# Kernel optimization log

Measured on AMD Instinct MI355X. Metric: run time of the kernel, lower is better.

## Reference

```python
import jax, jax.numpy as jnp
import numpy as np
from jax import lax

B, C, T, H, W = 4, 3, 2, 64, 64
DIM, HEADS, DH, MLP, DEPTH, SR, RES = 192, 3, 64, 768, 2, 2, 64
INNER = HEADS * DH  # 192 == DIM
N = RES * RES + 1   # 4097 tokens (cls + patches)


def setup_inputs() -> dict:
    key = jax.random.key(0)
    ks = iter(jax.random.split(key, 64))
    def rn(shape, s=0.02):
        return jax.random.normal(next(ks), shape, jnp.float32) * s
    d = {}
    d["x"] = jax.random.normal(next(ks), (B, C, T, H, W), jnp.float32)
    # patch embed conv3d (kernel (1,1,1) since patch_size=1) + layernorm
    d["pe_w"] = rn((DIM, C, 1, 1, 1))
    d["pe_b"] = jnp.zeros((DIM,), jnp.float32)
    d["pe_ln_g"] = jnp.ones((DIM,), jnp.float32)
    d["pe_ln_b"] = jnp.zeros((DIM,), jnp.float32)
    d["pos_emb"] = rn((1, T, N, DIM), 1.0)      # torch.randn
    d["space_token"] = rn((1, 1, DIM), 1.0)     # torch.randn
    ones2 = jnp.ones((DEPTH, DIM), jnp.float32)
    zeros2 = jnp.zeros((DEPTH, DIM), jnp.float32)
    # space transformer (Sattention with SR conv)
    d["s_ln1_g"], d["s_ln1_b"] = ones2, zeros2
    d["s_wq"] = rn((DEPTH, INNER, DIM))
    d["s_wkv"] = rn((DEPTH, 2 * INNER, DIM))
    d["s_wo"] = rn((DEPTH, DIM, INNER))
    d["s_bo"] = jnp.zeros((DEPTH, DIM), jnp.float32)
    d["s_sr_w"] = rn((DEPTH, DIM, DIM, SR, SR))
    d["s_sr_b"] = jnp.zeros((DEPTH, DIM), jnp.float32)
    d["s_ln2_g"], d["s_ln2_b"] = ones2, zeros2
    d["s_w1"] = rn((DEPTH, MLP, DIM))
    d["s_b1"] = jnp.zeros((DEPTH, MLP), jnp.float32)
    d["s_w2"] = rn((DEPTH, DIM, MLP))
    d["s_b2"] = jnp.zeros((DEPTH, DIM), jnp.float32)
    d["s_lnf_g"] = jnp.ones((DIM,), jnp.float32)
    d["s_lnf_b"] = jnp.zeros((DIM,), jnp.float32)
    # temporal transformer (plain attention over t=2 cls tokens)
    d["t_ln1_g"], d["t_ln1_b"] = ones2, zeros2
    d["t_wqkv"] = rn((DEPTH, 3 * INNER, DIM))
    d["t_wo"] = rn((DEPTH, DIM, INNER))
    d["t_bo"] = jnp.zeros((DEPTH, DIM), jnp.float32)
    d["t_ln2_g"], d["t_ln2_b"] = ones2, zeros2
    d["t_w1"] = rn((DEPTH, MLP, DIM))
    d["t_b1"] = jnp.zeros((DEPTH, MLP), jnp.float32)
    d["t_w2"] = rn((DEPTH, DIM, MLP))
    d["t_b2"] = jnp.zeros((DEPTH, DIM), jnp.float32)
    d["t_lnf_g"] = jnp.ones((DIM,), jnp.float32)
    d["t_lnf_b"] = jnp.zeros((DIM,), jnp.float32)
    return d


def _ln(x, g, b, eps=1e-5):
    m = jnp.mean(x, -1, keepdims=True)
    v = jnp.var(x, -1, keepdims=True)
    return (x - m) * lax.rsqrt(v + eps) * g + b


def _heads(t):
    b, n, _ = t.shape
    return t.reshape(b, n, HEADS, DH).transpose(0, 2, 1, 3)  # b h n d


def _attend(q, k, v):
    dots = jnp.einsum('bhid,bhjd->bhij', q, k) * (DH ** -0.5)
    attn = jax.nn.softmax(dots, axis=-1)
    o = jnp.einsum('bhij,bhjd->bhid', attn, v)
    return o.transpose(0, 2, 1, 3).reshape(q.shape[0], q.shape[2], INNER)


def _ff(x, w1, b1, w2, b2):
    h = jax.nn.gelu(x @ w1.T + b1, approximate=False)
    return h @ w2.T + b2


def _sattn(x, wq, wkv, wo, bo, srw, srb):
    bn = x.shape[0]
    q = _heads(x @ wq.T)
    # spatial reduction of non-cls tokens: b n d -> b d h w, conv stride SR
    xs = x[:, 1:].transpose(0, 2, 1).reshape(bn, DIM, RES, RES)
    xs = lax.conv_general_dilated(xs, srw, (SR, SR), 'VALID',
                                  dimension_numbers=('NCHW', 'OIHW', 'NCHW'))
    xs = xs + srb[None, :, None, None]
    xs = xs.reshape(bn, DIM, -1).transpose(0, 2, 1)
    xk = jnp.concatenate([x[:, :1], xs], axis=1)   # prepend cls token
    kv = xk @ wkv.T
    k, v = _heads(kv[..., :INNER]), _heads(kv[..., INNER:])
    return _attend(q, k, v) @ wo.T + bo


def _attn(x, wqkv, wo, bo):
    qkv = x @ wqkv.T
    q = _heads(qkv[..., :INNER])
    k = _heads(qkv[..., INNER:2 * INNER])
    v = _heads(qkv[..., 2 * INNER:])
    return _attend(q, k, v) @ wo.T + bo


def reference(x, pe_w, pe_b, pe_ln_g, pe_ln_b, pos_emb, space_token,
              s_ln1_g, s_ln1_b, s_wq, s_wkv, s_wo, s_bo, s_sr_w, s_sr_b,
              s_ln2_g, s_ln2_b, s_w1, s_b1, s_w2, s_b2, s_lnf_g, s_lnf_b,
              t_ln1_g, t_ln1_b, t_wqkv, t_wo, t_bo, t_ln2_g, t_ln2_b,
              t_w1, t_b1, t_w2, t_b2, t_lnf_g, t_lnf_b):
    # patch embed: (b,c,t,h,w) -> (b,t,hw,dim) with layernorm
    y = lax.conv_general_dilated(x, pe_w, (1, 1, 1), 'VALID',
                                 dimension_numbers=('NCDHW', 'OIDHW', 'NCDHW'))
    y = y + pe_b[None, :, None, None, None]
    y = jnp.transpose(y, (0, 2, 3, 4, 1)).reshape(B, T, RES * RES, DIM)
    y = _ln(y, pe_ln_g, pe_ln_b)
    cls = jnp.broadcast_to(space_token[:, None], (B, T, 1, DIM))
    xx = jnp.concatenate([cls, y], axis=2) + pos_emb[:, :, :N]
    xx = xx.reshape(B * T, N, DIM)
    for i in range(DEPTH):
        xx = _sattn(_ln(xx, s_ln1_g[i], s_ln1_b[i]), s_wq[i], s_wkv[i],
                    s_wo[i], s_bo[i], s_sr_w[i], s_sr_b[i]) + xx
        xx = _ff(_ln(xx, s_ln2_g[i], s_ln2_b[i]), s_w1[i], s_b1[i],
                 s_w2[i], s_b2[i]) + xx
    xx = _ln(xx, s_lnf_g, s_lnf_b)
    out = xx[:, 1:].reshape(B, T, RES, RES, DIM)
    z = xx[:, 0].reshape(B, T, DIM)
    for i in range(DEPTH):
        z = _attn(_ln(z, t_ln1_g[i], t_ln1_b[i]), t_wqkv[i], t_wo[i], t_bo[i]) + z
        z = _ff(_ln(z, t_ln2_g[i], t_ln2_b[i]), t_w1[i], t_b1[i], t_w2[i], t_b2[i]) + z
    z = _ln(z, t_lnf_g, t_lnf_b)
    return out + out * z[:, :, None, None, :]
```

## Files before the change

kernel.cpp:

```cpp
#include <hip/hip_runtime.h>
#include <hip/hip_bf16.h>
#include <math.h>

typedef __hip_bfloat16 bf16;
typedef short bf16x8 __attribute__((ext_vector_type(8)));
typedef float f32x4  __attribute__((ext_vector_type(4)));

#define BATCH 4
#define TT 2
#define BT 8
#define DIM 192
#define NTOK 4097
#define NKTOK 1025
#define HEADS 3
#define DH 64
#define MLPD 768
#define RES 64

__device__ __forceinline__ float b2f(bf16 v) { return __bfloat162float(v); }

__device__ __forceinline__ float rload(const void* p, size_t i, int flag) {
    if (flag) return __bfloat162float(((const bf16*)p)[i]);
    return ((const float*)p)[i];
}

__global__ void detect_kernel(const void* probe, int* flag) {
    unsigned u = *(const unsigned*)probe;
    *flag = (u == 0x3F800000u) ? 0 : 1;
}

__device__ __forceinline__ float blk_reduce_192(float v, float* tmp) {
    #pragma unroll
    for (int m = 32; m > 0; m >>= 1) v += __shfl_xor(v, m, 64);
    int wid = threadIdx.x >> 6;
    if ((threadIdx.x & 63) == 0) tmp[wid] = v;
    __syncthreads();
    float s = tmp[0] + tmp[1] + tmp[2];
    __syncthreads();
    return s;
}

__global__ void patch_embed_kernel(const void* __restrict__ x, const void* __restrict__ pe_w,
                                   const void* __restrict__ pe_b, const void* __restrict__ lng,
                                   const void* __restrict__ lnb, const void* __restrict__ pos,
                                   const void* __restrict__ st, float* __restrict__ XX,
                                   const int* __restrict__ dflag) {
    __shared__ float tmp[3];
    int flag = *dflag;
    int blk = blockIdx.x;
    int bt = blk / NTOK, n = blk % NTOK;
    int b = bt >> 1, t = bt & 1;
    int d = threadIdx.x;
    float val;
    if (n == 0) {
        val = rload(st, d, flag);
    } else {
        int p = n - 1, h = p >> 6, w = p & 63;
        size_t base = (size_t)(b * 6 + t) * 4096 + h * 64 + w;
        float conv = rload(pe_b, d, flag);
        #pragma unroll
        for (int c = 0; c < 3; ++c)
            conv += rload(x, base + (size_t)c * TT * 4096, flag) * rload(pe_w, d * 3 + c, flag);
        float s = blk_reduce_192(conv, tmp);
        float mean = s * (1.f / 192.f);
        float dv = conv - mean;
        float s2 = blk_reduce_192(dv * dv, tmp);
        float var = s2 * (1.f / 192.f);
        val = dv * rsqrtf(var + 1e-5f) * rload(lng, d, flag) + rload(lnb, d, flag);
    }
    val += rload(pos, ((size_t)t * NTOK + n) * DIM + d, flag);
    XX[(size_t)blk * DIM + d] = val;
}

__global__ void ln_bf16_kernel(const float* __restrict__ X, const void* __restrict__ g,
                               const void* __restrict__ b, size_t goff, bf16* __restrict__ Y,
                               const int* __restrict__ dflag) {
    __shared__ float tmp[3];
    int flag = *dflag;
    size_t row = blockIdx.x;
    int d = threadIdx.x;
    float v = X[row * DIM + d];
    float s = blk_reduce_192(v, tmp);
    float mean = s * (1.f / 192.f);
    float dv = v - mean;
    float s2 = blk_reduce_192(dv * dv, tmp);
    float var = s2 * (1.f / 192.f);
    Y[row * DIM + d] = __float2bfloat16(dv * rsqrtf(var + 1e-5f) * rload(g, goff + d, flag)
                                        + rload(b, goff + d, flag));
}

__global__ void ln_f32_kernel(const float* __restrict__ X, const void* __restrict__ g,
                              const void* __restrict__ b, size_t goff, float* __restrict__ Y,
                              long in_stride, const int* __restrict__ dflag) {
    __shared__ float tmp[3];
    int flag = *dflag;
    int d = threadIdx.x;
    float v = X[(size_t)blockIdx.x * in_stride + d];
    float s = blk_reduce_192(v, tmp);
    float mean = s * (1.f / 192.f);
    float dv = v - mean;
    float s2 = blk_reduce_192(dv * dv, tmp);
    float var = s2 * (1.f / 192.f);
    Y[(size_t)blockIdx.x * DIM + d] = dv * rsqrtf(var + 1e-5f) * rload(g, goff + d, flag)
                                      + rload(b, goff + d, flag);
}

__global__ __launch_bounds__(256) void gemm_mfma_kernel(
        const bf16* __restrict__ A, const void* __restrict__ W, size_t woff,
        const void* __restrict__ bias, size_t boff, const float* __restrict__ resid,
        float* __restrict__ Cf, bf16* __restrict__ Cb,
        int M, int N, int K, int do_gelu, const int* __restrict__ dflag) {
    __shared__ __align__(16) bf16 As[64 * 32];
    __shared__ __align__(16) bf16 Bs[64 * 32];
    int flag = *dflag;
    int tid = threadIdx.x;
    int wave = tid >> 6, lane = tid & 63;
    int quad = lane >> 4, l16 = lane & 15;
    int rowBase = blockIdx.y * 64;
    int colBase = blockIdx.x * 64;
    int srow = tid >> 2, scol = (tid & 3) * 8;

    f32x4 acc0 = {0.f, 0.f, 0.f, 0.f};
    f32x4 acc1 = acc0, acc2 = acc0, acc3 = acc0;

    for (int k0 = 0; k0 < K; k0 += 32) {
        {
            int gr = rowBase + srow;
            uint4 v = make_uint4(0u, 0u, 0u, 0u);
            if (gr < M) v = *reinterpret_cast<const uint4*>(A + (size_t)gr * K + k0 + scol);
            *reinterpret_cast<uint4*>(&As[srow * 32 + scol]) = v;
        }
        {
            int gr = colBase + srow;
            if (flag) {
                uint4 v = *reinterpret_cast<const uint4*>((const bf16*)W + woff + (size_t)gr * K + k0 + scol);
                *reinterpret_cast<uint4*>(&Bs[srow * 32 + scol]) = v;
            } else {
                const float* wp = (const float*)W + woff + (size_t)gr * K + k0 + scol;
                bf16 tmp8[8];
                #pragma unroll
                for (int j = 0; j < 8; ++j) tmp8[j] = __float2bfloat16(wp[j]);
                *reinterpret_cast<uint4*>(&Bs[srow * 32 + scol]) = *reinterpret_cast<uint4*>(tmp8);
            }
        }
        __syncthreads();
        bf16x8 af = *reinterpret_cast<bf16x8*>(&As[(wave * 16 + l16) * 32 + quad * 8]);
        bf16x8 bf0 = *reinterpret_cast<bf16x8*>(&Bs[(0 * 16 + l16) * 32 + quad * 8]);
        bf16x8 bf1 = *reinterpret_cast<bf16x8*>(&Bs[(1 * 16 + l16) * 32 + quad * 8]);
        bf16x8 bf2 = *reinterpret_cast<bf16x8*>(&Bs[(2 * 16 + l16) * 32 + quad * 8]);
        bf16x8 bf3 = *reinterpret_cast<bf16x8*>(&Bs[(3 * 16 + l16) * 32 + quad * 8]);
        acc0 = __builtin_amdgcn_mfma_f32_16x16x32_bf16(af, bf0, acc0, 0, 0, 0);
        acc1 = __builtin_amdgcn_mfma_f32_16x16x32_bf16(af, bf1, acc1, 0, 0, 0);
        acc2 = __builtin_amdgcn_mfma_f32_16x16x32_bf16(af, bf2, acc2, 0, 0, 0);
        acc3 = __builtin_amdgcn_mfma_f32_16x16x32_bf16(af, bf3, acc3, 0, 0, 0);
        __syncthreads();
    }

    f32x4 accs[4] = {acc0, acc1, acc2, acc3};
    #pragma unroll
    for (int t = 0; t < 4; ++t) {
        int col = colBase + t * 16 + l16;
        float bv = bias ? rload(bias, boff + col, flag) : 0.f;
        #pragma unroll
        for (int r = 0; r < 4; ++r) {
            int row = rowBase + wave * 16 + quad * 4 + r;
            if (row < M) {
                float v = accs[t][r] + bv;
                if (do_gelu) v = 0.5f * v * (1.f + erff(v * 0.70710678118654752f));
                if (resid) v += resid[(size_t)row * N + col];
                if (Cf) Cf[(size_t)row * N + col] = v;
                else    Cb[(size_t)row * N + col] = __float2bfloat16(v);
            }
        }
    }
}

__global__ void gemm_fA_kernel(const float* __restrict__ A, const void* __restrict__ W,
                               size_t woff, const void* __restrict__ bias, size_t boff,
                               const float* __restrict__ resid, float* __restrict__ C,
                               int M, int N, int K, int do_gelu, const int* __restrict__ dflag) {
    __shared__ float As[16][17];
    __shared__ float Ws[16][17];
    int flag = *dflag;
    int tx = threadIdx.x, ty = threadIdx.y;
    int row = blockIdx.y * 16 + ty;
    int col = blockIdx.x * 16 + tx;
    float acc = 0.f;
    for (int k0 = 0; k0 < K; k0 += 16) {
        As[ty][tx] = (row < M) ? A[(size_t)row * K + k0 + tx] : 0.f;
        int wr = blockIdx.x * 16 + ty;
        Ws[ty][tx] = (wr < N) ? rload(W, woff + (size_t)wr * K + k0 + tx, flag) : 0.f;
        __syncthreads();
        #pragma unroll
        for (int kk = 0; kk < 16; ++kk)
            acc += As[ty][kk] * Ws[tx][kk];
        __syncthreads();
    }
    if (row < M && col < N) {
        float v = acc;
        if (bias) v += rload(bias, boff + col, flag);
        if (do_gelu) v = 0.5f * v * (1.f + erff(v * 0.70710678118654752f));
        if (resid) v += resid[(size_t)row * N + col];
        C[(size_t)row * N + col] = v;
    }
}

__global__ void copy_cls_kernel(const bf16* __restrict__ AB, bf16* __restrict__ XK) {
    int bt = blockIdx.x, d = threadIdx.x;
    XK[(size_t)bt * NKTOK * DIM + d] = AB[(size_t)bt * NTOK * DIM + d];
}

__global__ void wtrans_kernel(const void* __restrict__ srw, bf16* __restrict__ WT,
                              const int* __restrict__ dflag) {
    int flag = *dflag;
    int idx = blockIdx.x * 256 + threadIdx.x;
    int i = idx / (192 * 768);
    int rem = idx - i * (192 * 768);
    int dout = rem / 768;
    int kp = rem - dout * 768;
    int q = kp / 192, c = kp - q * 192;
    size_t src = ((size_t)(i * 192 + dout) * 192 + c) * 4 + q;
    WT[idx] = __float2bfloat16(rload(srw, src, flag));
}

__global__ __launch_bounds__(256) void srconv_mfma_kernel(
        const bf16* __restrict__ XLN, const bf16* __restrict__ WT, size_t woff,
        const void* __restrict__ bias, size_t boff, bf16* __restrict__ XK,
        const int* __restrict__ dflag) {
    __shared__ __align__(16) bf16 As[64 * 32];
    __shared__ __align__(16) bf16 Bs[64 * 32];
    int flag = *dflag;
    int tid = threadIdx.x;
    int wave = tid >> 6, lane = tid & 63;
    int quad = lane >> 4, l16 = lane & 15;
    int rowBase = blockIdx.y * 64;
    int colBase = blockIdx.x * 64;
    int srow = tid >> 2, scol = (tid & 3) * 8;

    int arow = rowBase + srow;
    int abt = arow >> 10, apos = arow & 1023;
    int aoh = apos >> 5, aow = apos & 31;

    f32x4 acc0 = {0.f, 0.f, 0.f, 0.f};
    f32x4 acc1 = acc0, acc2 = acc0, acc3 = acc0;

    for (int k0 = 0; k0 < 768; k0 += 32) {
        int q = k0 / 192, c0 = k0 - q * 192;
        int kh = q >> 1, kw = q & 1;
        int n = 1 + ((2 * aoh + kh) << 6) + (2 * aow + kw);
        {
            uint4 v = *reinterpret_cast<const uint4*>(
                XLN + ((size_t)abt * NTOK + n) * DIM + c0 + scol);
            *reinterpret_cast<uint4*>(&As[srow * 32 + scol]) = v;
        }
        {
            int gr = colBase + srow;
            uint4 v = *reinterpret_cast<const uint4*>(WT + woff + (size_t)gr * 768 + k0 + scol);
            *reinterpret_cast<uint4*>(&Bs[srow * 32 + scol]) = v;
        }
        __syncthreads();
        bf16x8 af = *reinterpret_cast<bf16x8*>(&As[(wave * 16 + l16) * 32 + quad * 8]);
        bf16x8 bf0 = *reinterpret_cast<bf16x8*>(&Bs[(0 * 16 + l16) * 32 + quad * 8]);
        bf16x8 bf1 = *reinterpret_cast<bf16x8*>(&Bs[(1 * 16 + l16) * 32 + quad * 8]);
        bf16x8 bf2 = *reinterpret_cast<bf16x8*>(&Bs[(2 * 16 + l16) * 32 + quad * 8]);
        bf16x8 bf3 = *reinterpret_cast<bf16x8*>(&Bs[(3 * 16 + l16) * 32 + quad * 8]);
        acc0 = __builtin_amdgcn_mfma_f32_16x16x32_bf16(af, bf0, acc0, 0, 0, 0);
        acc1 = __builtin_amdgcn_mfma_f32_16x16x32_bf16(af, bf1, acc1, 0, 0, 0);
        acc2 = __builtin_amdgcn_mfma_f32_16x16x32_bf16(af, bf2, acc2, 0, 0, 0);
        acc3 = __builtin_amdgcn_mfma_f32_16x16x32_bf16(af, bf3, acc3, 0, 0, 0);
        __syncthreads();
    }

    f32x4 accs[4] = {acc0, acc1, acc2, acc3};
    #pragma unroll
    for (int t = 0; t < 4; ++t) {
        int col = colBase + t * 16 + l16;
        float bv = rload(bias, boff + col, flag);
        #pragma unroll
        for (int r = 0; r < 4; ++r) {
            int row = rowBase + wave * 16 + quad * 4 + r;
            int bt = row >> 10, pos = row & 1023;
            XK[((size_t)bt * NKTOK + 1 + pos) * DIM + col] = __float2bfloat16(accs[t][r] + bv);
        }
    }
}

__global__ __launch_bounds__(256) void sattn_mfma_kernel(const bf16* __restrict__ Q,
                                                         const bf16* __restrict__ KV,
                                                         bf16* __restrict__ O) {
    __shared__ __align__(16) bf16 Ks[32 * 72];
    __shared__ __align__(16) bf16 Vts[64 * 36];
    __shared__ __align__(16) bf16 Ps[4][16 * 68];

    int bt = blockIdx.x / HEADS, h = blockIdx.x % HEADS;
    int q0 = blockIdx.y * 64;
    int tid = threadIdx.x;
    int wave = tid >> 6, lane = tid & 63;
    int quad = lane >> 4, l16 = lane & 15;

    int qrow = q0 + wave * 16 + l16;
    int qr = (qrow < NTOK) ? qrow : (NTOK - 1);
    const bf16* qp = Q + ((size_t)bt * NTOK + qr) * DIM + h * DH + quad * 8;
    bf16x8 aq0 = *reinterpret_cast<const bf16x8*>(qp);
    bf16x8 aq1 = *reinterpret_cast<const bf16x8*>(qp + 32);

    float l_r[4] = {0.f, 0.f, 0.f, 0.f};
    f32x4 O0 = {0.f, 0.f, 0.f, 0.f}, O1 = O0, O2 = O0, O3 = O0;

    int skey = tid & 31, sdh0 = (tid >> 5) * 8;
    union U8 { bf16x8 v; uint2 u[2]; };

    for (int kt0 = 0; kt0 < NKTOK; kt0 += 32) {
        __syncthreads();
        {
            int gkey = kt0 + skey;
            uint4 kv4 = make_uint4(0u, 0u, 0u, 0u), vv4 = make_uint4(0u, 0u, 0u, 0u);
            if (gkey < NKTOK) {
                const bf16* kp = KV + ((size_t)bt * NKTOK + gkey) * (2 * DIM) + h * DH + sdh0;
                kv4 = *reinterpret_cast<const uint4*>(kp);
                vv4 = *reinterpret_cast<const uint4*>(kp + DIM);
            }
            *reinterpret_cast<uint2*>(&Ks[skey * 72 + sdh0])     = make_uint2(kv4.x, kv4.y);
            *reinterpret_cast<uint2*>(&Ks[skey * 72 + sdh0 + 4]) = make_uint2(kv4.z, kv4.w);
            const bf16* vb = reinterpret_cast<const bf16*>(&vv4);
            #pragma unroll
            for (int j = 0; j < 8; ++j) Vts[(sdh0 + j) * 36 + skey] = vb[j];
        }
        __syncthreads();

        f32x4 S[2];
        #pragma unroll
        for (int sub = 0; sub < 2; ++sub) {
            U8 k0c, k1c;
            const bf16* kr = &Ks[(sub * 16 + l16) * 72 + quad * 8];
            k0c.u[0] = *reinterpret_cast<const uint2*>(kr);
            k0c.u[1] = *reinterpret_cast<const uint2*>(kr + 4);
            const bf16* kr2 = kr + 32;
            k1c.u[0] = *reinterpret_cast<const uint2*>(kr2);
            k1c.u[1] = *reinterpret_cast<const uint2*>(kr2 + 4);
            f32x4 z = {0.f, 0.f, 0.f, 0.f};
            z = __builtin_amdgcn_mfma_f32_16x16x32_bf16(aq0, k0c.v, z, 0, 0, 0);
            z = __builtin_amdgcn_mfma_f32_16x16x32_bf16(aq1, k1c.v, z, 0, 0, 0);
            S[sub] = z;
        }

        bool oob0 = (kt0 + l16) >= NKTOK;
        bool oob1 = (kt0 + 16 + l16) >= NKTOK;
        #pragma unroll
        for (int r = 0; r < 4; ++r) {
            float p0 = oob0 ? 0.f : __expf(S[0][r] * 0.125f);
            float p1 = oob1 ? 0.f : __expf(S[1][r] * 0.125f);
            l_r[r] += p0 + p1;
            Ps[wave][(quad * 4 + r) * 68 + l16]      = __float2bfloat16(p0);
            Ps[wave][(quad * 4 + r) * 68 + 16 + l16] = __float2bfloat16(p1);
        }

        U8 pa;
        const bf16* pp = &Ps[wave][l16 * 68 + quad * 8];
        pa.u[0] = *reinterpret_cast<const uint2*>(pp);
        pa.u[1] = *reinterpret_cast<const uint2*>(pp + 4);
        U8 vf[4];
        #pragma unroll
        for (int t = 0; t < 4; ++t) {
            const bf16* vp = &Vts[(t * 16 + l16) * 36 + quad * 8];
            vf[t].u[0] = *reinterpret_cast<const uint2*>(vp);
            vf[t].u[1] = *reinterpret_cast<const uint2*>(vp + 4);
        }
        O0 = __builtin_amdgcn_mfma_f32_16x16x32_bf16(pa.v, vf[0].v, O0, 0, 0, 0);
        O1 = __builtin_amdgcn_mfma_f32_16x16x32_bf16(pa.v, vf[1].v, O1, 0, 0, 0);
        O2 = __builtin_amdgcn_mfma_f32_16x16x32_bf16(pa.v, vf[2].v, O2, 0, 0, 0);
        O3 = __builtin_amdgcn_mfma_f32_16x16x32_bf16(pa.v, vf[3].v, O3, 0, 0, 0);
    }

    #pragma unroll
    for (int r = 0; r < 4; ++r) {
        #pragma unroll
        for (int msk = 1; msk < 16; msk <<= 1)
            l_r[r] += __shfl_xor(l_r[r], msk, 64);
    }

    f32x4 Os[4] = {O0, O1, O2, O3};
    #pragma unroll
    for (int r = 0; r < 4; ++r) {
        int row = q0 + wave * 16 + quad * 4 + r;
        if (row < NTOK) {
            float inv = 1.f / l_r[r];
            bf16* op = O + ((size_t)bt * NTOK + row) * DIM + h * DH + l16;
            #pragma unroll
            for (int t = 0; t < 4; ++t)
                op[t * 16] = __float2bfloat16(Os[t][r] * inv);
        }
    }
}

__global__ void tattn_kernel(const float* __restrict__ QKV, float* __restrict__ O) {
    int b = blockIdx.x / HEADS, h = blockIdx.x % HEADS;
    int d = threadIdx.x;
    int r0 = b * 2, r1 = b * 2 + 1;
    float q0 = QKV[r0 * 576 + h * DH + d];
    float q1 = QKV[r1 * 576 + h * DH + d];
    float k0 = QKV[r0 * 576 + 192 + h * DH + d];
    float k1 = QKV[r1 * 576 + 192 + h * DH + d];
    float v0 = QKV[r0 * 576 + 384 + h * DH + d];
    float v1 = QKV[r1 * 576 + 384 + h * DH + d];
    float s00 = q0 * k0, s01 = q0 * k1, s10 = q1 * k0, s11 = q1 * k1;
    #pragma unroll
    for (int mm = 32; mm > 0; mm >>= 1) {
        s00 += __shfl_xor(s00, mm, 64);
        s01 += __shfl_xor(s01, mm, 64);
        s10 += __shfl_xor(s10, mm, 64);
        s11 += __shfl_xor(s11, mm, 64);
    }
    s00 *= 0.125f; s01 *= 0.125f; s10 *= 0.125f; s11 *= 0.125f;
    float m0 = fmaxf(s00, s01), m1 = fmaxf(s10, s11);
    float e00 = expf(s00 - m0), e01 = expf(s01 - m0);
    float e10 = expf(s10 - m1), e11 = expf(s11 - m1);
    float i0 = 1.f / (e00 + e01), i1 = 1.f / (e10 + e11);
    O[r0 * DIM + h * DH + d] = (e00 * v0 + e01 * v1) * i0;
    O[r1 * DIM + h * DH + d] = (e10 * v0 + e11 * v1) * i1;
}

__global__ void final_kernel(const float* __restrict__ XX, const void* __restrict__ g,
                             const void* __restrict__ b, const float* __restrict__ ZF,
                             void* __restrict__ out, const int* __restrict__ dflag) {
    __shared__ float tmp[3];
    int flag = *dflag;
    int tok = blockIdx.x;
    int bt = tok >> 12, p = tok & 4095;
    int d = threadIdx.x;
    size_t row = (size_t)bt * NTOK + 1 + p;
    float v = XX[row * DIM + d];
    float s = blk_reduce_192(v, tmp);
    float mean = s * (1.f / 192.f);
    float dv = v - mean;
    float s2 = blk_reduce_192(dv * dv, tmp);
    float var = s2 * (1.f / 192.f);
    float ln = dv * rsqrtf(var + 1e-5f) * rload(g, d, flag) + rload(b, d, flag);
    float o = ln * (1.f + ZF[bt * DIM + d]);
    size_t oi = (size_t)tok * DIM + d;
    if (flag) ((bf16*)out)[oi] = __float2bfloat16(o);
    else      ((float*)out)[oi] = o;
}

extern "C" void kernel_launch(void* const* d_in, const int* in_sizes, int n_in,
                              void* d_out, int out_size, void* d_ws, size_t ws_size,
                              hipStream_t stream) {
    const void* x       = d_in[0];
    const void* pe_w    = d_in[1];
    const void* pe_b    = d_in[2];
    const void* pe_ln_g = d_in[3];
    const void* pe_ln_b = d_in[4];
    const void* pos_emb = d_in[5];
    const void* space_t = d_in[6];
    const void* s_ln1_g = d_in[7];
    const void* s_ln1_b = d_in[8];
    const void* s_wq    = d_in[9];
    const void* s_wkv   = d_in[10];
    const void* s_wo    = d_in[11];
    const void* s_bo    = d_in[12];
    const void* s_sr_w  = d_in[13];
    const void* s_sr_b  = d_in[14];
    const void* s_ln2_g = d_in[15];
    const void* s_ln2_b = d_in[16];
    const void* s_w1    = d_in[17];
    const void* s_b1    = d_in[18];
    const void* s_w2    = d_in[19];
    const void* s_b2    = d_in[20];
    const void* s_lnf_g = d_in[21];
    const void* s_lnf_b = d_in[22];
    const void* t_ln1_g = d_in[23];
    const void* t_ln1_b = d_in[24];
    const void* t_wqkv  = d_in[25];
    const void* t_wo    = d_in[26];
    const void* t_bo    = d_in[27];
    const void* t_ln2_g = d_in[28];
    const void* t_ln2_b = d_in[29];
    const void* t_w1    = d_in[30];
    const void* t_b1    = d_in[31];
    const void* t_w2    = d_in[32];
    const void* t_b2    = d_in[33];
    const void* t_lnf_g = d_in[34];
    const void* t_lnf_b = d_in[35];

    const int M  = BT * NTOK;
    const int MK = BT * NKTOK;
    const int CHROWS = 8194;

    char* base = (char*)d_ws;
    int* dflag = (int*)base;
    size_t off = 256;
    auto carve = [&](size_t bytes) -> void* {
        void* p = base + off;
        off += (bytes + 255) & ~(size_t)255;
        return p;
    };
    float* XX = (float*)carve((size_t)M * DIM * 4);
    bf16*  AB = (bf16*) carve((size_t)M * DIM * 2);
    bf16*  QH = (bf16*) carve((size_t)M * DIM * 2);
    bf16*  XK = (bf16*) carve((size_t)MK * DIM * 2);
    bf16*  KV = (bf16*) carve((size_t)MK * 2 * DIM * 2);
    bf16*  WT = (bf16*) carve((size_t)2 * DIM * 768 * 2);
    float* Z    = (float*)carve(BT * DIM * 4);
    float* ZLN  = (float*)carve(BT * DIM * 4);
    float* ZQKV = (float*)carve(BT * 576 * 4);
    float* ZATT = (float*)carve(BT * DIM * 4);
    float* ZH   = (float*)carve(BT * MLPD * 4);
    float* ZF   = (float*)carve(BT * DIM * 4);

    dim3 g16(16, 16);

    detect_kernel<<<1, 1, 0, stream>>>(pe_ln_g, dflag);
    wtrans_kernel<<<(2 * 192 * 768) / 256, 256, 0, stream>>>(s_sr_w, WT, dflag);
    patch_embed_kernel<<<M, DIM, 0, stream>>>(x, pe_w, pe_b, pe_ln_g, pe_ln_b,
                                              pos_emb, space_t, XX, dflag);

    for (int i = 0; i < 2; ++i) {
        size_t oLN  = (size_t)i * DIM;
        size_t oWQ  = (size_t)i * DIM * DIM;
        size_t oWKV = (size_t)i * 2 * DIM * DIM;
        size_t oWO  = (size_t)i * DIM * DIM;
        size_t oWT  = (size_t)i * DIM * 768;
        size_t oW1  = (size_t)i * MLPD * DIM;
        size_t oB1  = (size_t)i * MLPD;
        size_t oW2  = (size_t)i * DIM * MLPD;

        ln_bf16_kernel<<<M, DIM, 0, stream>>>(XX, s_ln1_g, s_ln1_b, oLN, AB, dflag);
        gemm_mfma_kernel<<<dim3(DIM / 64, (M + 63) / 64), 256, 0, stream>>>(
            AB, s_wq, oWQ, nullptr, 0, nullptr, nullptr, QH, M, DIM, DIM, 0, dflag);
        copy_cls_kernel<<<BT, DIM, 0, stream>>>(AB, XK);
        srconv_mfma_kernel<<<dim3(DIM / 64, (BT * 1024) / 64), 256, 0, stream>>>(
            AB, WT, oWT, s_sr_b, oLN, XK, dflag);
        gemm_mfma_kernel<<<dim3(2 * DIM / 64, (MK + 63) / 64), 256, 0, stream>>>(
            XK, s_wkv, oWKV, nullptr, 0, nullptr, nullptr, KV, MK, 2 * DIM, DIM, 0, dflag);
        sattn_mfma_kernel<<<dim3(BT * HEADS, (NTOK + 63) / 64), 256, 0, stream>>>(QH, KV, AB);
        gemm_mfma_kernel<<<dim3(DIM / 64, (M + 63) / 64), 256, 0, stream>>>(
            AB, s_wo, oWO, s_bo, oLN, XX, XX, nullptr, M, DIM, DIM, 0, dflag);
        ln_bf16_kernel<<<M, DIM, 0, stream>>>(XX, s_ln2_g, s_ln2_b, oLN, AB, dflag);
        for (int c = 0; c < 4; ++c) {
            size_t aoff = (size_t)c * CHROWS * DIM;
            gemm_mfma_kernel<<<dim3(MLPD / 64, (CHROWS + 63) / 64), 256, 0, stream>>>(
                AB + aoff, s_w1, oW1, s_b1, oB1, nullptr, nullptr, QH, CHROWS, MLPD, DIM, 1, dflag);
            gemm_mfma_kernel<<<dim3(DIM / 64, (CHROWS + 63) / 64), 256, 0, stream>>>(
                QH, s_w2, oW2, s_b2, oLN, XX + aoff, XX + aoff, nullptr, CHROWS, DIM, MLPD, 0, dflag);
        }
    }

    ln_f32_kernel<<<BT, DIM, 0, stream>>>(XX, s_lnf_g, s_lnf_b, 0, Z, (long)((size_t)NTOK * DIM), dflag);
    for (int i = 0; i < 2; ++i) {
        size_t oLN   = (size_t)i * DIM;
        size_t oWQKV = (size_t)i * 3 * DIM * DIM;
        size_t oWO   = (size_t)i * DIM * DIM;
        size_t oW1   = (size_t)i * MLPD * DIM;
        size_t oB1   = (size_t)i * MLPD;
        size_t oW2   = (size_t)i * DIM * MLPD;
        ln_f32_kernel<<<BT, DIM, 0, stream>>>(Z, t_ln1_g, t_ln1_b, oLN, ZLN, DIM, dflag);
        gemm_fA_kernel<<<dim3(576 / 16, 1), g16, 0, stream>>>(
            ZLN, t_wqkv, oWQKV, nullptr, 0, nullptr, ZQKV, BT, 576, DIM, 0, dflag);
        tattn_kernel<<<BATCH * HEADS, 64, 0, stream>>>(ZQKV, ZATT);
        gemm_fA_kernel<<<dim3(DIM / 16, 1), g16, 0, stream>>>(
            ZATT, t_wo, oWO, t_bo, oLN, Z, Z, BT, DIM, DIM, 0, dflag);
        ln_f32_kernel<<<BT, DIM, 0, stream>>>(Z, t_ln2_g, t_ln2_b, oLN, ZLN, DIM, dflag);
        gemm_fA_kernel<<<dim3(MLPD / 16, 1), g16, 0, stream>>>(
            ZLN, t_w1, oW1, t_b1, oB1, nullptr, ZH, BT, MLPD, DIM, 1, dflag);
        gemm_fA_kernel<<<dim3(DIM / 16, 1), g16, 0, stream>>>(
            ZH, t_w2, oW2, t_b2, oLN, Z, Z, BT, DIM, MLPD, 0, dflag);
    }
    ln_f32_kernel<<<BT, DIM, 0, stream>>>(Z, t_lnf_g, t_lnf_b, 0, ZF, DIM, dflag);

    final_kernel<<<BT * 4096, DIM, 0, stream>>>(XX, s_lnf_g, s_lnf_b, ZF, d_out, dflag);
}
```

Before: 1.029 ms.

## Fuse temporal transformer into one kernel and use wave-per-row layernorms

Replaces the chain of small temporal-transformer launches (layernorms, tiled fp32 GEMMs, attention) with one single-block kernel. That kernel keeps the 8 cls-token rows in shared memory and streams the weights with 8-wide vector loads. Layernorm, patch-embed and final kernels now process one row per 64-wide wave, four rows per block, with shuffle-only reductions, which removes the shared-memory reductions and __syncthreads. The goal is lower launch overhead and better occupancy, at the cost of running the temporal weight streaming on a single CU.

```diff
diff --git a/kernel.cpp b/kernel.cpp
--- a/kernel.cpp
+++ b/kernel.cpp
@@ -24,85 +24,103 @@
     return ((const float*)p)[i];
 }
 
+__device__ __forceinline__ void unpack8(uint4 u, float* f) {
+    unsigned w[4] = {u.x, u.y, u.z, u.w};
+    #pragma unroll
+    for (int k = 0; k < 4; ++k) {
+        union { unsigned u; float f; } a, b;
+        a.u = (w[k] & 0xFFFFu) << 16;
+        b.u = w[k] & 0xFFFF0000u;
+        f[2 * k] = a.f;
+        f[2 * k + 1] = b.f;
+    }
+}
+
+__device__ __forceinline__ void wload8(const void* W, size_t i, int flag, float* f) {
+    if (flag) {
+        uint4 u = *reinterpret_cast<const uint4*>((const bf16*)W + i);
+        unpack8(u, f);
+    } else {
+        const float* p = (const float*)W + i;
+        #pragma unroll
+        for (int j = 0; j < 8; ++j) f[j] = p[j];
+    }
+}
+
 __global__ void detect_kernel(const void* probe, int* flag) {
     unsigned u = *(const unsigned*)probe;
     *flag = (u == 0x3F800000u) ? 0 : 1;
 }
 
-__device__ __forceinline__ float blk_reduce_192(float v, float* tmp) {
-    #pragma unroll
-    for (int m = 32; m > 0; m >>= 1) v += __shfl_xor(v, m, 64);
-    int wid = threadIdx.x >> 6;
-    if ((threadIdx.x & 63) == 0) tmp[wid] = v;
-    __syncthreads();
-    float s = tmp[0] + tmp[1] + tmp[2];
-    __syncthreads();
-    return s;
-}
-
-__global__ void patch_embed_kernel(const void* __restrict__ x, const void* __restrict__ pe_w,
-                                   const void* __restrict__ pe_b, const void* __restrict__ lng,
-                                   const void* __restrict__ lnb, const void* __restrict__ pos,
-                                   const void* __restrict__ st, float* __restrict__ XX,
-                                   const int* __restrict__ dflag) {
-    __shared__ float tmp[3];
+__global__ __launch_bounds__(256) void patch_embed4_kernel(
+        const void* __restrict__ x, const void* __restrict__ pe_w,
+        const void* __restrict__ pe_b, const void* __restrict__ lng,
+        const void* __restrict__ lnb, const void* __restrict__ pos,
+        const void* __restrict__ st, float* __restrict__ XX,
+        const int* __restrict__ dflag) {
     int flag = *dflag;
-    int blk = blockIdx.x;
-    int bt = blk / NTOK, n = blk % NTOK;
+    int w = threadIdx.x >> 6, lane = threadIdx.x & 63;
+    int row = blockIdx.x * 4 + w;
+    int bt = row / NTOK, n = row % NTOK;
     int b = bt >> 1, t = bt & 1;
-    int d = threadIdx.x;
-    float val;
+    int d0 = lane, d1 = lane + 64, d2 = lane + 128;
+    float o0, o1, o2;
     if (n == 0) {
-        val = rload(st, d, flag);
+        o0 = rload(st, d0, flag); o1 = rload(st, d1, flag); o2 = rload(st, d2, flag);
     } else {
-        int p = n - 1, h = p >> 6, w = p & 63;
-        size_t base = (size_t)(b * 6 + t) * 4096 + h * 64 + w;
-        float conv = rload(pe_b, d, flag);
-        #pragma unroll
-        for (int c = 0; c < 3; ++c)
-            conv += rload(x, base + (size_t)c * TT * 4096, flag) * rload(pe_w, d * 3 + c, flag);
-        float s = blk_reduce_192(conv, tmp);
+        int p = n - 1, hh = p >> 6, ww = p & 63;
+        size_t base = (size_t)(b * 6 + t) * 4096 + hh * 64 + ww;
+        float xv0 = rload(x, base, flag);
+        float xv1 = rload(x, base + (size_t)TT * 4096, flag);
+        float xv2 = rload(x, base + (size_t)2 * TT * 4096, flag);
+        float c0 = rload(pe_b, d0, flag) + xv0 * rload(pe_w, d0 * 3, flag)
+                 + xv1 * rload(pe_w, d0 * 3 + 1, flag) + xv2 * rload(pe_w, d0 * 3 + 2, flag);
+        float c1 = rload(pe_b, d1, flag) + xv0 * rload(pe_w, d1 * 3, flag)
+                 + xv1 * rload(pe_w, d1 * 3 + 1, flag) + xv2 * rload(pe_w, d1 * 3 + 2, flag);
+        float c2 = rload(pe_b, d2, flag) + xv0 * rload(pe_w, d2 * 3, flag)
+                 + xv1 * rload(pe_w, d2 * 3 + 1, flag) + xv2 * rload(pe_w, d2 * 3 + 2, flag);
+        float s = c0 + c1 + c2;
+        #pragma unroll
+        for (int m = 32; m > 0; m >>= 1) s += __shfl_xor(s, m, 64);
         float mean = s * (1.f / 192.f);
-        float dv = conv - mean;
-        float s2 = blk_reduce_192(dv * dv, tmp);
-        float var = s2 * (1.f / 192.f);
-        val = dv * rsqrtf(var + 1e-5f) * rload(lng, d, flag) + rload(lnb, d, flag);
-    }
-    val += rload(pos, ((size_t)t * NTOK + n) * DIM + d, flag);
-    XX[(size_t)blk * DIM + d] = val;
-}
-
-__global__ void ln_bf16_kernel(const float* __restrict__ X, const void* __restrict__ g,
-                               const void* __restrict__ b, size_t goff, bf16* __restrict__ Y,
-                               const int* __restrict__ dflag) {
-    __shared__ float tmp[3];
+        float e0 = c0 - mean, e1 = c1 - mean, e2 = c2 - mean;
+        float s2 = e0 * e0 + e1 * e1 + e2 * e2;
+        #pragma unroll
+        for (int m = 32; m > 0; m >>= 1) s2 += __shfl_xor(s2, m, 64);
+        float inv = rsqrtf(s2 * (1.f / 192.f) + 1e-5f);
+        o0 = e0 * inv * rload(lng, d0, flag) + rload(lnb, d0, flag);
+        o1 = e1 * inv * rload(lng, d1, flag) + rload(lnb, d1, flag);
+        o2 = e2 * inv * rload(lng, d2, flag) + rload(lnb, d2, flag);
+    }
+    size_t pbase = ((size_t)t * NTOK + n) * DIM;
+    o0 += rload(pos, pbase + d0, flag);
+    o1 += rload(pos, pbase + d1, flag);
+    o2 += rload(pos, pbase + d2, flag);
+    float* xp = XX + (size_t)row * DIM;
+    xp[d0] = o0; xp[d1] = o1; xp[d2] = o2;
+}
+
+__global__ __launch_bounds__(256) void ln4_kernel(const float* __restrict__ X,
+        const void* __restrict__ g, const void* __restrict__ b, size_t goff,
+        bf16* __restrict__ Y, const int* __restrict__ dflag) {
     int flag = *dflag;
-    size_t row = blockIdx.x;
-    int d = threadIdx.x;
-    float v = X[row * DIM + d];
-    float s = blk_reduce_192(v, tmp);
+    int w = threadIdx.x >> 6, lane = threadIdx.x & 63;
+    size_t row = (size_t)blockIdx.x * 4 + w;
+    const float* xp = X + row * DIM;
+    float v0 = xp[lane], v1 = xp[lane + 64], v2 = xp[lane + 128];
+    float s = v0 + v1 + v2;
+    #pragma unroll
+    for (int m = 32; m > 0; m >>= 1) s += __shfl_xor(s, m, 64);
     float mean = s * (1.f / 192.f);
-    float dv = v - mean;
-    float s2 = blk_reduce_192(dv * dv, tmp);
-    float var = s2 * (1.f / 192.f);
-    Y[row * DIM + d] = __float2bfloat16(dv * rsqrtf(var + 1e-5f) * rload(g, goff + d, flag)
-                                        + rload(b, goff + d, flag));
-}
-
-__global__ void ln_f32_kernel(const float* __restrict__ X, const void* __restrict__ g,
-                              const void* __restrict__ b, size_t goff, float* __restrict__ Y,
-                              long in_stride, const int* __restrict__ dflag) {
-    __shared__ float tmp[3];
-    int flag = *dflag;
-    int d = threadIdx.x;
-    float v = X[(size_t)blockIdx.x * in_stride + d];
-    float s = blk_reduce_192(v, tmp);
-    float mean = s * (1.f / 192.f);
-    float dv = v - mean;
-    float s2 = blk_reduce_192(dv * dv, tmp);
-    float var = s2 * (1.f / 192.f);
-    Y[(size_t)blockIdx.x * DIM + d] = dv * rsqrtf(var + 1e-5f) * rload(g, goff + d, flag)
-                                      + rload(b, goff + d, flag);
+    float e0 = v0 - mean, e1 = v1 - mean, e2 = v2 - mean;
+    float s2 = e0 * e0 + e1 * e1 + e2 * e2;
+    #pragma unroll
+    for (int m = 32; m > 0; m >>= 1) s2 += __shfl_xor(s2, m, 64);
+    float inv = rsqrtf(s2 * (1.f / 192.f) + 1e-5f);
+    bf16* yp = Y + row * DIM;
+    yp[lane]       = __float2bfloat16(e0 * inv * rload(g, goff + lane, flag)       + rload(b, goff + lane, flag));
+    yp[lane + 64]  = __float2bfloat16(e1 * inv * rload(g, goff + lane + 64, flag)  + rload(b, goff + lane + 64, flag));
+    yp[lane + 128] = __float2bfloat16(e2 * inv * rload(g, goff + lane + 128, flag) + rload(b, goff + lane + 128, flag));
 }
 
 __global__ __launch_bounds__(256) void gemm_mfma_kernel(
@@ -175,36 +193,6 @@
     }
 }
 
-__global__ void gemm_fA_kernel(const float* __restrict__ A, const void* __restrict__ W,
-                               size_t woff, const void* __restrict__ bias, size_t boff,
-                               const float* __restrict__ resid, float* __restrict__ C,
-                               int M, int N, int K, int do_gelu, const int* __restrict__ dflag) {
-    __shared__ float As[16][17];
-    __shared__ float Ws[16][17];
-    int flag = *dflag;
-    int tx = threadIdx.x, ty = threadIdx.y;
-    int row = blockIdx.y * 16 + ty;
-    int col = blockIdx.x * 16 + tx;
-    float acc = 0.f;
-    for (int k0 = 0; k0 < K; k0 += 16) {
-        As[ty][tx] = (row < M) ? A[(size_t)row * K + k0 + tx] : 0.f;
-        int wr = blockIdx.x * 16 + ty;
-        Ws[ty][tx] = (wr < N) ? rload(W, woff + (size_t)wr * K + k0 + tx, flag) : 0.f;
-        __syncthreads();
-        #pragma unroll
-        for (int kk = 0; kk < 16; ++kk)
-            acc += As[ty][kk] * Ws[tx][kk];
-        __syncthreads();
-    }
-    if (row < M && col < N) {
-        float v = acc;
-        if (bias) v += rload(bias, boff + col, flag);
-        if (do_gelu) v = 0.5f * v * (1.f + erff(v * 0.70710678118654752f));
-        if (resid) v += resid[(size_t)row * N + col];
-        C[(size_t)row * N + col] = v;
-    }
-}
-
 __global__ void copy_cls_kernel(const bf16* __restrict__ AB, bf16* __restrict__ XK) {
     int bt = blockIdx.x, d = threadIdx.x;
     XK[(size_t)bt * NKTOK * DIM + d] = AB[(size_t)bt * NTOK * DIM + d];
@@ -393,53 +381,207 @@
     }
 }
 
-__global__ void tattn_kernel(const float* __restrict__ QKV, float* __restrict__ O) {
-    int b = blockIdx.x / HEADS, h = blockIdx.x % HEADS;
-    int d = threadIdx.x;
-    int r0 = b * 2, r1 = b * 2 + 1;
-    float q0 = QKV[r0 * 576 + h * DH + d];
-    float q1 = QKV[r1 * 576 + h * DH + d];
-    float k0 = QKV[r0 * 576 + 192 + h * DH + d];
-    float k1 = QKV[r1 * 576 + 192 + h * DH + d];
-    float v0 = QKV[r0 * 576 + 384 + h * DH + d];
-    float v1 = QKV[r1 * 576 + 384 + h * DH + d];
-    float s00 = q0 * k0, s01 = q0 * k1, s10 = q1 * k0, s11 = q1 * k1;
-    #pragma unroll
-    for (int mm = 32; mm > 0; mm >>= 1) {
-        s00 += __shfl_xor(s00, mm, 64);
-        s01 += __shfl_xor(s01, mm, 64);
-        s10 += __shfl_xor(s10, mm, 64);
-        s11 += __shfl_xor(s11, mm, 64);
-    }
-    s00 *= 0.125f; s01 *= 0.125f; s10 *= 0.125f; s11 *= 0.125f;
-    float m0 = fmaxf(s00, s01), m1 = fmaxf(s10, s11);
-    float e00 = expf(s00 - m0), e01 = expf(s01 - m0);
-    float e10 = expf(s10 - m1), e11 = expf(s11 - m1);
-    float i0 = 1.f / (e00 + e01), i1 = 1.f / (e10 + e11);
-    O[r0 * DIM + h * DH + d] = (e00 * v0 + e01 * v1) * i0;
-    O[r1 * DIM + h * DH + d] = (e10 * v0 + e11 * v1) * i1;
-}
-
-__global__ void final_kernel(const float* __restrict__ XX, const void* __restrict__ g,
-                             const void* __restrict__ b, const float* __restrict__ ZF,
-                             void* __restrict__ out, const int* __restrict__ dflag) {
-    __shared__ float tmp[3];
+__global__ __launch_bounds__(256) void temporal_fused_kernel(
+        const float* __restrict__ XX,
+        const void* lnf_g, const void* lnf_b,
+        const void* ln1_g, const void* ln1_b, const void* wqkv,
+        const void* wo, const void* bo, const void* ln2_g, const void* ln2_b,
+        const void* w1, const void* b1, const void* w2, const void* b2,
+        const void* tlnf_g, const void* tlnf_b,
+        float* __restrict__ ZF, const int* __restrict__ dflag) {
+    __shared__ float Zs[8 * 192];
+    __shared__ float B1[8 * 192];
+    __shared__ float B2[8 * 768];
+    __shared__ float Sc[12][4];
     int flag = *dflag;
-    int tok = blockIdx.x;
+    int tid = threadIdx.x;
+    int g = tid >> 5, l32 = tid & 31;
+
+    auto ln_row = [&](const float* src, long stride, float* dst, const void* gg,
+                      const void* bb, size_t goff) {
+        const float* xp = src + (size_t)g * stride;
+        float v[6];
+        float s = 0.f;
+        #pragma unroll
+        for (int j = 0; j < 6; ++j) { v[j] = xp[l32 + 32 * j]; s += v[j]; }
+        #pragma unroll
+        for (int m = 16; m > 0; m >>= 1) s += __shfl_xor(s, m, 32);
+        float mean = s * (1.f / 192.f);
+        float s2 = 0.f;
+        #pragma unroll
+        for (int j = 0; j < 6; ++j) { float dv = v[j] - mean; s2 += dv * dv; }
+        #pragma unroll
+        for (int m = 16; m > 0; m >>= 1) s2 += __shfl_xor(s2, m, 32);
+        float inv = rsqrtf(s2 * (1.f / 192.f) + 1e-5f);
+        #pragma unroll
+        for (int j = 0; j < 6; ++j) {
+            int d = l32 + 32 * j;
+            dst[g * 192 + d] = (v[j] - mean) * inv * rload(gg, goff + d, flag)
+                               + rload(bb, goff + d, flag);
+        }
+    };
+
+    ln_row(XX, (long)NTOK * DIM, Zs, lnf_g, lnf_b, 0);
+    __syncthreads();
+
+    for (int i = 0; i < 2; ++i) {
+        size_t oLN   = (size_t)i * DIM;
+        size_t oWQKV = (size_t)i * 3 * DIM * DIM;
+        size_t oWO   = (size_t)i * DIM * DIM;
+        size_t oW1   = (size_t)i * MLPD * DIM;
+        size_t oB1   = (size_t)i * MLPD;
+        size_t oW2   = (size_t)i * DIM * MLPD;
+
+        ln_row(Zs, 192, B1, ln1_g, ln1_b, oLN);
+        __syncthreads();
+
+        for (int n = tid; n < 576; n += 256) {
+            float acc[8] = {0.f, 0.f, 0.f, 0.f, 0.f, 0.f, 0.f, 0.f};
+            for (int k = 0; k < 192; k += 8) {
+                float wf[8];
+                wload8(wqkv, oWQKV + (size_t)n * 192 + k, flag, wf);
+                #pragma unroll
+                for (int j = 0; j < 8; ++j)
+                    #pragma unroll
+                    for (int r = 0; r < 8; ++r)
+                        acc[r] += B1[r * 192 + k + j] * wf[j];
+            }
+            #pragma unroll
+            for (int r = 0; r < 8; ++r) B2[r * 576 + n] = acc[r];
+        }
+        __syncthreads();
+
+        if (tid < 12) {
+            int b = tid / 3, h = tid % 3;
+            int r0 = 2 * b, r1 = r0 + 1;
+            float s00 = 0.f, s01 = 0.f, s10 = 0.f, s11 = 0.f;
+            for (int d = 0; d < 64; ++d) {
+                float q0 = B2[r0 * 576 + h * 64 + d];
+                float q1 = B2[r1 * 576 + h * 64 + d];
+                float k0 = B2[r0 * 576 + 192 + h * 64 + d];
+                float k1 = B2[r1 * 576 + 192 + h * 64 + d];
+                s00 += q0 * k0; s01 += q0 * k1; s10 += q1 * k0; s11 += q1 * k1;
+            }
+            Sc[tid][0] = s00 * 0.125f; Sc[tid][1] = s01 * 0.125f;
+            Sc[tid][2] = s10 * 0.125f; Sc[tid][3] = s11 * 0.125f;
+        }
+        __syncthreads();
+
+        for (int idx = tid; idx < 768; idx += 256) {
+            int p = idx >> 6, d = idx & 63;
+            int b = p / 3, h = p % 3;
+            int r0 = 2 * b, r1 = r0 + 1;
+            float s00 = Sc[p][0], s01 = Sc[p][1], s10 = Sc[p][2], s11 = Sc[p][3];
+            float m0 = fmaxf(s00, s01), m1 = fmaxf(s10, s11);
+            float e00 = __expf(s00 - m0), e01 = __expf(s01 - m0);
+            float e10 = __expf(s10 - m1), e11 = __expf(s11 - m1);
+            float i0 = 1.f / (e00 + e01), i1 = 1.f / (e10 + e11);
+            float v0 = B2[r0 * 576 + 384 + h * 64 + d];
+            float v1 = B2[r1 * 576 + 384 + h * 64 + d];
+            B1[r0 * 192 + h * 64 + d] = (e00 * v0 + e01 * v1) * i0;
+            B1[r1 * 192 + h * 64 + d] = (e10 * v0 + e11 * v1) * i1;
+        }
+        __syncthreads();
+
+        if (tid < 192) {
+            int n = tid;
+            float bv = rload(bo, oLN + n, flag);
+            float acc[8] = {bv, bv, bv, bv, bv, bv, bv, bv};
+            for (int k = 0; k < 192; k += 8) {
+                float wf[8];
+                wload8(wo, oWO + (size_t)n * 192 + k, flag, wf);
+                #pragma unroll
+                for (int j = 0; j < 8; ++j)
+                    #pragma unroll
+                    for (int r = 0; r < 8; ++r)
+                        acc[r] += B1[r * 192 + k + j] * wf[j];
+            }
+            #pragma unroll
+            for (int r = 0; r < 8; ++r) Zs[r * 192 + n] += acc[r];
+        }
+        __syncthreads();
+
+        ln_row(Zs, 192, B1, ln2_g, ln2_b, oLN);
+        __syncthreads();
+
+        for (int n = tid; n < 768; n += 256) {
+            float bv = rload(b1, oB1 + n, flag);
+            float acc[8] = {bv, bv, bv, bv, bv, bv, bv, bv};
+            for (int k = 0; k < 192; k += 8) {
+                float wf[8];
+                wload8(w1, oW1 + (size_t)n * 192 + k, flag, wf);
+                #pragma unroll
+                for (int j = 0; j < 8; ++j)
+                    #pragma unroll
+                    for (int r = 0; r < 8; ++r)
+                        acc[r] += B1[r * 192 + k + j] * wf[j];
+            }
+            #pragma unroll
+            for (int r = 0; r < 8; ++r) {
+                float v = acc[r];
+                B2[r * 768 + n] = 0.5f * v * (1.f + erff(v * 0.70710678118654752f));
+            }
+        }
+        __syncthreads();
+
+        if (tid < 192) {
+            int n = tid;
+            float bv = rload(b2, oLN + n, flag);
+            float acc[8] = {bv, bv, bv, bv, bv, bv, bv, bv};
+            for (int k = 0; k < 768; k += 8) {
+                float wf[8];
+                wload8(w2, oW2 + (size_t)n * 768 + k, flag, wf);
+                #pragma unroll
+                for (int j = 0; j < 8; ++j)
+                    #pragma unroll
+                    for (int r = 0; r < 8; ++r)
+                        acc[r] += B2[r * 768 + k + j] * wf[j];
+            }
+            #pragma unroll
+            for (int r = 0; r < 8; ++r) Zs[r * 192 + n] += acc[r];
+        }
+        __syncthreads();
+    }
+
+    ln_row(Zs, 192, B1, tlnf_g, tlnf_b, 0);
+    __syncthreads();
+    for (int idx = tid; idx < 8 * 192; idx += 256) ZF[idx] = B1[idx];
+}
+
+__global__ __launch_bounds__(256) void final4_kernel(const float* __restrict__ XX,
+        const void* __restrict__ g, const void* __restrict__ b,
+        const float* __restrict__ ZF, void* __restrict__ out,
+        const int* __restrict__ dflag) {
+    int flag = *dflag;
+    int w = threadIdx.x >> 6, lane = threadIdx.x & 63;
+    int tok = blockIdx.x * 4 + w;
     int bt = tok >> 12, p = tok & 4095;
-    int d = threadIdx.x;
     size_t row = (size_t)bt * NTOK + 1 + p;
-    float v = XX[row * DIM + d];
-    float s = blk_reduce_192(v, tmp);
+    const float* xp = XX + row * DIM;
+    float v0 = xp[lane], v1 = xp[lane + 64], v2 = xp[lane + 128];
+    float s = v0 + v1 + v2;
+    #pragma unroll
+    for (int m = 32; m > 0; m >>= 1) s += __shfl_xor(s, m, 64);
     float mean = s * (1.f / 192.f);
-    float dv = v - mean;
-    float s2 = blk_reduce_192(dv * dv, tmp);
-    float var = s2 * (1.f / 192.f);
-    float ln = dv * rsqrtf(var + 1e-5f) * rload(g, d, flag) + rload(b, d, flag);
-    float o = ln * (1.f + ZF[bt * DIM + d]);
-    size_t oi = (size_t)tok * DIM + d;
-    if (flag) ((bf16*)out)[oi] = __float2bfloat16(o);
-    else      ((float*)out)[oi] = o;
+    float e0 = v0 - mean, e1 = v1 - mean, e2 = v2 - mean;
+    float s2 = e0 * e0 + e1 * e1 + e2 * e2;
+    #pragma unroll
+    for (int m = 32; m > 0; m >>= 1) s2 += __shfl_xor(s2, m, 64);
+    float inv = rsqrtf(s2 * (1.f / 192.f) + 1e-5f);
+    const float* zp = ZF + bt * DIM;
+    float o0 = (e0 * inv * rload(g, lane, flag)       + rload(b, lane, flag))       * (1.f + zp[lane]);
+    float o1 = (e1 * inv * rload(g, lane + 64, flag)  + rload(b, lane + 64, flag))  * (1.f + zp[lane + 64]);
+    float o2 = (e2 * inv * rload(g, lane + 128, flag) + rload(b, lane + 128, flag)) * (1.f + zp[lane + 128]);
+    size_t ob = (size_t)tok * DIM;
+    if (flag) {
+        bf16* op = (bf16*)out + ob;
+        op[lane] = __float2bfloat16(o0);
+        op[lane + 64] = __float2bfloat16(o1);
+        op[lane + 128] = __float2bfloat16(o2);
+    } else {
+        float* op = (float*)out + ob;
+        op[lane] = o0; op[lane + 64] = o1; op[lane + 128] = o2;
+    }
 }
 
 extern "C" void kernel_launch(void* const* d_in, const int* in_sizes, int n_in,
@@ -500,19 +642,12 @@
     bf16*  XK = (bf16*) carve((size_t)MK * DIM * 2);
     bf16*  KV = (bf16*) carve((size_t)MK * 2 * DIM * 2);
     bf16*  WT = (bf16*) carve((size_t)2 * DIM * 768 * 2);
-    float* Z    = (float*)carve(BT * DIM * 4);
-    float* ZLN  = (float*)carve(BT * DIM * 4);
-    float* ZQKV = (float*)carve(BT * 576 * 4);
-    float* ZATT = (float*)carve(BT * DIM * 4);
-    float* ZH   = (float*)carve(BT * MLPD * 4);
-    float* ZF   = (float*)carve(BT * DIM * 4);
-
-    dim3 g16(16, 16);
+    float* ZF = (float*)carve(BT * DIM * 4);
 
     detect_kernel<<<1, 1, 0, stream>>>(pe_ln_g, dflag);
     wtrans_kernel<<<(2 * 192 * 768) / 256, 256, 0, stream>>>(s_sr_w, WT, dflag);
-    patch_embed_kernel<<<M, DIM, 0, stream>>>(x, pe_w, pe_b, pe_ln_g, pe_ln_b,
-                                              pos_emb, space_t, XX, dflag);
+    patch_embed4_kernel<<<M / 4, 256, 0, stream>>>(x, pe_w, pe_b, pe_ln_g, pe_ln_b,
+                                                   pos_emb, space_t, XX, dflag);
 
     for (int i = 0; i < 2; ++i) {
         size_t oLN  = (size_t)i * DIM;
@@ -524,7 +659,7 @@
         size_t oB1  = (size_t)i * MLPD;
         size_t oW2  = (size_t)i * DIM * MLPD;
 
-        ln_bf16_kernel<<<M, DIM, 0, stream>>>(XX, s_ln1_g, s_ln1_b, oLN, AB, dflag);
+        ln4_kernel<<<M / 4, 256, 0, stream>>>(XX, s_ln1_g, s_ln1_b, oLN, AB, dflag);
         gemm_mfma_kernel<<<dim3(DIM / 64, (M + 63) / 64), 256, 0, stream>>>(
             AB, s_wq, oWQ, nullptr, 0, nullptr, nullptr, QH, M, DIM, DIM, 0, dflag);
         copy_cls_kernel<<<BT, DIM, 0, stream>>>(AB, XK);
@@ -535,7 +670,7 @@
         sattn_mfma_kernel<<<dim3(BT * HEADS, (NTOK + 63) / 64), 256, 0, stream>>>(QH, KV, AB);
         gemm_mfma_kernel<<<dim3(DIM / 64, (M + 63) / 64), 256, 0, stream>>>(
             AB, s_wo, oWO, s_bo, oLN, XX, XX, nullptr, M, DIM, DIM, 0, dflag);
-        ln_bf16_kernel<<<M, DIM, 0, stream>>>(XX, s_ln2_g, s_ln2_b, oLN, AB, dflag);
+        ln4_kernel<<<M / 4, 256, 0, stream>>>(XX, s_ln2_g, s_ln2_b, oLN, AB, dflag);
         for (int c = 0; c < 4; ++c) {
             size_t aoff = (size_t)c * CHROWS * DIM;
             gemm_mfma_kernel<<<dim3(MLPD / 64, (CHROWS + 63) / 64), 256, 0, stream>>>(
@@ -545,27 +680,9 @@
         }
     }
 
-    ln_f32_kernel<<<BT, DIM, 0, stream>>>(XX, s_lnf_g, s_lnf_b, 0, Z, (long)((size_t)NTOK * DIM), dflag);
-    for (int i = 0; i < 2; ++i) {
-        size_t oLN   = (size_t)i * DIM;
-        size_t oWQKV = (size_t)i * 3 * DIM * DIM;
-        size_t oWO   = (size_t)i * DIM * DIM;
-        size_t oW1   = (size_t)i * MLPD * DIM;
-        size_t oB1   = (size_t)i * MLPD;
-        size_t oW2   = (size_t)i * DIM * MLPD;
-        ln_f32_kernel<<<BT, DIM, 0, stream>>>(Z, t_ln1_g, t_ln1_b, oLN, ZLN, DIM, dflag);
-        gemm_fA_kernel<<<dim3(576 / 16, 1), g16, 0, stream>>>(
-            ZLN, t_wqkv, oWQKV, nullptr, 0, nullptr, ZQKV, BT, 576, DIM, 0, dflag);
-        tattn_kernel<<<BATCH * HEADS, 64, 0, stream>>>(ZQKV, ZATT);
-        gemm_fA_kernel<<<dim3(DIM / 16, 1), g16, 0, stream>>>(
-            ZATT, t_wo, oWO, t_bo, oLN, Z, Z, BT, DIM, DIM, 0, dflag);
-        ln_f32_kernel<<<BT, DIM, 0, stream>>>(Z, t_ln2_g, t_ln2_b, oLN, ZLN, DIM, dflag);
-        gemm_fA_kernel<<<dim3(MLPD / 16, 1), g16, 0, stream>>>(
-            ZLN, t_w1, oW1, t_b1, oB1, nullptr, ZH, BT, MLPD, DIM, 1, dflag);
-        gemm_fA_kernel<<<dim3(DIM / 16, 1), g16, 0, stream>>>(
-            ZH, t_w2, oW2, t_b2, oLN, Z, Z, BT, DIM, MLPD, 0, dflag);
-    }
-    ln_f32_kernel<<<BT, DIM, 0, stream>>>(Z, t_lnf_g, t_lnf_b, 0, ZF, DIM, dflag);
-
-    final_kernel<<<BT * 4096, DIM, 0, stream>>>(XX, s_lnf_g, s_lnf_b, ZF, d_out, dflag);
-}
+    temporal_fused_kernel<<<1, 256, 0, stream>>>(
+        XX, s_lnf_g, s_lnf_b, t_ln1_g, t_ln1_b, t_wqkv, t_wo, t_bo,
+        t_ln2_g, t_ln2_b, t_w1, t_b1, t_w2, t_b2, t_lnf_g, t_lnf_b, ZF, dflag);
+
+    final4_kernel<<<(BT * 4096) / 4, 256, 0, stream>>>(XX, s_lnf_g, s_lnf_b, ZF, d_out, dflag);
+}
```

Result: slower. 1.110 ms (+7.8%).
